# Kernel optimization log

Measured on AMD Instinct MI355X. Metric: run time of the kernel, lower is better.

## Reference

```python
import jax, jax.numpy as jnp
import numpy as np


def setup_inputs() -> dict:
    key = jax.random.key(0)
    k1, k2, k3, k4 = jax.random.split(key, 4)
    N, D, E = 100000, 128, 600000
    inputs = jax.random.normal(k1, (N, D), dtype=jnp.float32)
    r_indices = jax.random.randint(k2, (E,), 0, N, dtype=jnp.int64)
    c_indices = jax.random.randint(k3, (E,), 0, N, dtype=jnp.int64)
    W = jax.random.normal(k4, (D, 1), dtype=jnp.float32) * (1.0 / np.sqrt(D))
    b = jnp.zeros((1,), dtype=jnp.float32)
    return {"inputs": inputs, "r_indices": r_indices, "c_indices": c_indices, "W": W, "b": b}


def reference(inputs, r_indices, c_indices, W, b):
    # dropout rate is 1 - self.dropout = 0 -> identity
    row = inputs[r_indices]          # [E, D] gather
    col = inputs[c_indices]          # [E, D] gather
    diff = jnp.abs(row - col)        # [E, D]
    return diff @ W + b              # [E, 1] Dense(1) edge score
```

## Files before the change

kernel.cpp:

```cpp
#include <hip/hip_runtime.h>

#define WAVES_PER_BLOCK 4
#define U 8

__global__ __launch_bounds__(256) void edge_score_kernel(
    const float* __restrict__ inputs,
    const int*   __restrict__ r_idx,
    const int*   __restrict__ c_idx,
    const float* __restrict__ W,
    const float* __restrict__ bias_p,
    float*       __restrict__ out,
    int E)
{
    const int lane   = threadIdx.x & 63;
    const int wid    = threadIdx.x >> 6;
    const int gwave  = blockIdx.x * WAVES_PER_BLOCK + wid;
    const int nwaves = gridDim.x * WAVES_PER_BLOCK;

    const float2 w    = ((const float2*)W)[lane];
    const float  bias = bias_p[0];

    const int Efull = E & ~(U - 1);

    for (int e0 = gwave * U; e0 < Efull; e0 += nwaves * U) {
        int r[U], c[U];
        #pragma unroll
        for (int i = 0; i < U; ++i) {
            r[i] = r_idx[e0 + i];
            c[i] = c_idx[e0 + i];
        }
        float2 a[U], b[U];
        #pragma unroll
        for (int i = 0; i < U; ++i) {
            a[i] = ((const float2*)(inputs + (size_t)r[i] * 128))[lane];
            b[i] = ((const float2*)(inputs + (size_t)c[i] * 128))[lane];
        }

        float p[U];
        #pragma unroll
        for (int i = 0; i < U; ++i)
            p[i] = fabsf(a[i].x - b[i].x) * w.x + fabsf(a[i].y - b[i].y) * w.y;

        #pragma unroll
        for (int off = 32; off > 0; off >>= 1) {
            #pragma unroll
            for (int i = 0; i < U; ++i)
                p[i] += __shfl_xor(p[i], off, 64);
        }

        float v = p[0];
        #pragma unroll
        for (int i = 1; i < U; ++i)
            v = (lane == i) ? p[i] : v;
        if (lane < U) out[e0 + lane] = v + bias;
    }

    for (int e = Efull + gwave; e < E; e += nwaves) {
        const int rr = r_idx[e];
        const int cc = c_idx[e];
        const float2 a = ((const float2*)(inputs + (size_t)rr * 128))[lane];
        const float2 b = ((const float2*)(inputs + (size_t)cc * 128))[lane];
        float partial = fabsf(a.x - b.x) * w.x + fabsf(a.y - b.y) * w.y;
        #pragma unroll
        for (int off = 32; off > 0; off >>= 1)
            partial += __shfl_xor(partial, off, 64);
        if (lane == 0) out[e] = partial + bias;
    }
}

extern "C" void kernel_launch(void* const* d_in, const int* in_sizes, int n_in,
                              void* d_out, int out_size, void* d_ws, size_t ws_size,
                              hipStream_t stream) {
    const float* inputs = (const float*)d_in[0];
    const int*   r_idx  = (const int*)d_in[1];
    const int*   c_idx  = (const int*)d_in[2];
    const float* W      = (const float*)d_in[3];
    const float* b      = (const float*)d_in[4];
    float*       out    = (float*)d_out;

    const int E = in_sizes[1];

    const int blocks = 2048;
    edge_score_kernel<<<blocks, 256, 0, stream>>>(inputs, r_idx, c_idx, W, b, out, E);
}
```

Baseline: 163.4 us.

## Convert feature table to bf16 before gathering edge rows

Adds a pre-pass that converts the fp32 node feature table to bf16 in workspace, then gathers the bf16 rows in the edge kernel, halving the bytes per gathered row. The conversion reads 51MB and writes 25.6MB every call. The gather then moves 600k×2×256B instead of 512B per row. It also lowers numerical precision of the inputs, which may exceed tolerance. An fp32 fallback without unrolling is used if the workspace is too small.

After: 140.2 us. 1.17x faster.

```diff
diff --git a/kernel.cpp b/kernel.cpp
--- a/kernel.cpp
+++ b/kernel.cpp
@@ -3,8 +3,42 @@
 #define WAVES_PER_BLOCK 4
 #define U 8
 
-__global__ __launch_bounds__(256) void edge_score_kernel(
-    const float* __restrict__ inputs,
+
+__device__ inline unsigned short f2bf_rne(float f) {
+    unsigned u = __float_as_uint(f);
+    u += 0x7FFFu + ((u >> 16) & 1u);
+    return (unsigned short)(u >> 16);
+}
+
+__device__ inline float2 bf2_to_f2(unsigned u) {
+    float2 f;
+    f.x = __uint_as_float(u << 16);
+    f.y = __uint_as_float(u & 0xFFFF0000u);
+    return f;
+}
+
+
+__global__ __launch_bounds__(256) void convert_kernel(
+    const float* __restrict__ in,
+    unsigned short* __restrict__ out,
+    int n4)
+{
+    int i = blockIdx.x * blockDim.x + threadIdx.x;
+    const int stride = gridDim.x * blockDim.x;
+    for (; i < n4; i += stride) {
+        float4 v = ((const float4*)in)[i];
+        ushort4 o;
+        o.x = f2bf_rne(v.x);
+        o.y = f2bf_rne(v.y);
+        o.z = f2bf_rne(v.z);
+        o.w = f2bf_rne(v.w);
+        ((ushort4*)out)[i] = o;
+    }
+}
+
+
+__global__ __launch_bounds__(256) void edge_score_bf16_kernel(
+    const unsigned* __restrict__ table,
     const int*   __restrict__ r_idx,
     const int*   __restrict__ c_idx,
     const float* __restrict__ W,
@@ -29,17 +63,20 @@
             r[i] = r_idx[e0 + i];
             c[i] = c_idx[e0 + i];
         }
-        float2 a[U], b[U];
+        unsigned ua[U], ub[U];
         #pragma unroll
         for (int i = 0; i < U; ++i) {
-            a[i] = ((const float2*)(inputs + (size_t)r[i] * 128))[lane];
-            b[i] = ((const float2*)(inputs + (size_t)c[i] * 128))[lane];
+            ua[i] = table[(size_t)r[i] * 64 + lane];
+            ub[i] = table[(size_t)c[i] * 64 + lane];
         }
 
         float p[U];
         #pragma unroll
-        for (int i = 0; i < U; ++i)
-            p[i] = fabsf(a[i].x - b[i].x) * w.x + fabsf(a[i].y - b[i].y) * w.y;
+        for (int i = 0; i < U; ++i) {
+            float2 a = bf2_to_f2(ua[i]);
+            float2 b = bf2_to_f2(ub[i]);
+            p[i] = fabsf(a.x - b.x) * w.x + fabsf(a.y - b.y) * w.y;
+        }
 
         #pragma unroll
         for (int off = 32; off > 0; off >>= 1) {
@@ -58,8 +95,39 @@
     for (int e = Efull + gwave; e < E; e += nwaves) {
         const int rr = r_idx[e];
         const int cc = c_idx[e];
-        const float2 a = ((const float2*)(inputs + (size_t)rr * 128))[lane];
-        const float2 b = ((const float2*)(inputs + (size_t)cc * 128))[lane];
+        float2 a = bf2_to_f2(table[(size_t)rr * 64 + lane]);
+        float2 b = bf2_to_f2(table[(size_t)cc * 64 + lane]);
+        float partial = fabsf(a.x - b.x) * w.x + fabsf(a.y - b.y) * w.y;
+        #pragma unroll
+        for (int off = 32; off > 0; off >>= 1)
+            partial += __shfl_xor(partial, off, 64);
+        if (lane == 0) out[e] = partial + bias;
+    }
+}
+
+
+__global__ __launch_bounds__(256) void edge_score_f32_kernel(
+    const float* __restrict__ inputs,
+    const int*   __restrict__ r_idx,
+    const int*   __restrict__ c_idx,
+    const float* __restrict__ W,
+    const float* __restrict__ bias_p,
+    float*       __restrict__ out,
+    int E)
+{
+    const int lane   = threadIdx.x & 63;
+    const int wid    = threadIdx.x >> 6;
+    const int gwave  = blockIdx.x * WAVES_PER_BLOCK + wid;
+    const int nwaves = gridDim.x * WAVES_PER_BLOCK;
+
+    const float2 w    = ((const float2*)W)[lane];
+    const float  bias = bias_p[0];
+
+    for (int e = gwave; e < E; e += nwaves) {
+        const int r = r_idx[e];
+        const int c = c_idx[e];
+        const float2 a = ((const float2*)(inputs + (size_t)r * 128))[lane];
+        const float2 b = ((const float2*)(inputs + (size_t)c * 128))[lane];
         float partial = fabsf(a.x - b.x) * w.x + fabsf(a.y - b.y) * w.y;
         #pragma unroll
         for (int off = 32; off > 0; off >>= 1)
@@ -78,8 +146,18 @@
     const float* b      = (const float*)d_in[4];
     float*       out    = (float*)d_out;
 
-    const int E = in_sizes[1];
+    const int N_D = in_sizes[0];
+    const int E   = in_sizes[1];
 
-    const int blocks = 2048;
-    edge_score_kernel<<<blocks, 256, 0, stream>>>(inputs, r_idx, c_idx, W, b, out, E);
+    const size_t bf16_bytes = (size_t)N_D * 2;
+
+    if (ws_size >= bf16_bytes) {
+        unsigned short* table_bf16 = (unsigned short*)d_ws;
+        convert_kernel<<<2048, 256, 0, stream>>>(inputs, table_bf16, N_D / 4);
+        edge_score_bf16_kernel<<<2048, 256, 0, stream>>>(
+            (const unsigned*)table_bf16, r_idx, c_idx, W, b, out, E);
+    } else {
+        edge_score_f32_kernel<<<2048, 256, 0, stream>>>(
+            inputs, r_idx, c_idx, W, b, out, E);
+    }
 }
```
